# Optimization experiments

Hardware: AMD Instinct MI355X
Metric: run time of the kernel (lower is better)

The kernel has to match this reference:

```python
import jax, jax.numpy as jnp
import numpy as np

H = 64  # GRU hidden size


def _gru_scan(x_proj, m, U, b_rec):
    # x_proj: [S,B,3H] precomputed input projections (time-major); m: [S,B] bool mask
    B = x_proj.shape[1]
    h0 = jnp.zeros((B, H), x_proj.dtype)

    def step(h, inp):
        xp, mt = inp
        rec = h @ U + b_rec                       # [B,3H] (Keras reset_after=True)
        xz, xr, xh = jnp.split(xp, 3, axis=-1)
        rz, rr, rh = jnp.split(rec, 3, axis=-1)
        z = jax.nn.sigmoid(xz + rz)
        r = jax.nn.sigmoid(xr + rr)
        hh = jnp.tanh(xh + r * rh)
        hn = z * h + (1.0 - z) * hh
        hn = jnp.where(mt[:, None], hn, h)        # masked steps carry state through
        return hn, hn

    hT, hs = jax.lax.scan(step, h0, (x_proj, m))
    return hs, hT  # hs: [S,B,H], hT: [B,H]


def setup_inputs() -> dict:
    key = jax.random.key(0)
    ks = jax.random.split(key, 16)
    V, E = 50000, 25
    B, S, T = 512, 200, 10
    s = 0.05
    f32 = jnp.float32
    inp = {
        "input_batch": jax.random.randint(ks[0], (B, S, T), 0, V),
        "emb_table": jax.random.normal(ks[1], (V, E), f32) * s,
        "W_f": jax.random.normal(ks[2], (E, 3 * H), f32) * s,
        "U_f": jax.random.normal(ks[3], (H, 3 * H), f32) * s,
        "b_f": jnp.zeros((2, 3 * H), f32),
        "W_b": jax.random.normal(ks[4], (E, 3 * H), f32) * s,
        "U_b": jax.random.normal(ks[5], (H, 3 * H), f32) * s,
        "b_b": jnp.zeros((2, 3 * H), f32),
        "W_k": jax.random.normal(ks[6], (2 * H, H), f32) * s,
        "b_k": jnp.zeros((H,), f32),
        "W_q": jax.random.normal(ks[7], (H, H), f32) * s,
        "b_q": jnp.zeros((H,), f32),
        "W_e": jax.random.normal(ks[8], (H, 1), f32) * s,
        "b_e": jnp.zeros((1,), f32),
    }
    return inp


def reference(input_batch, emb_table, W_f, U_f, b_f, W_b, U_b, b_b, W_k, b_k, W_q, b_q, W_e, b_e):
    mask = input_batch != 0                                  # [B,S,T]
    emb = emb_table[input_batch]                             # [B,S,T,E]
    nm = mask.astype(emb.dtype)
    denom = nm.sum(axis=2)                                   # [B,S]
    denom = jnp.where(denom == 0, jnp.ones_like(denom), denom)
    x = (emb * nm[..., None]).sum(axis=2) / denom[..., None] # [B,S,E] masked mean over tags
    step_mask = mask[:, :, 0]                                # [B,S] GRU step mask

    xT = jnp.swapaxes(x, 0, 1)                               # [S,B,E]
    mT = jnp.swapaxes(step_mask, 0, 1)                       # [S,B]

    # forward GRU
    hs_f, hT_f = _gru_scan(xT @ W_f + b_f[0], mT, U_f, b_f[1])
    # backward GRU: reverse time, scan, reverse back
    hs_b, _ = _gru_scan((xT @ W_b + b_b[0])[::-1], mT[::-1], U_b, b_b[1])
    hs_b = hs_b[::-1]

    out = jnp.swapaxes(jnp.concatenate([hs_f, hs_b], axis=-1), 0, 1)  # [B,S,2H]

    # Bahdanau attention; query = forward final state
    keys = out @ W_k + b_k                                   # [B,S,H]
    queries = hT_f @ W_q + b_q                               # [B,H]
    e = jnp.tanh(keys + queries[:, None, :]) @ W_e + b_e     # [B,S,1]
    e = e + (1.0 - step_mask.astype(e.dtype))[..., None] * -1e9
    w = jax.nn.softmax(e, axis=1)                            # [B,S,1]
    context = (w * out).sum(axis=1)                          # [B,2H]
    return context
```

## Files before the change

### kernel.cpp

```cpp
#include <hip/hip_runtime.h>
#include <math.h>

#define BATCH 512
#define SEQ   200
#define TOK   10
#define EMB   25
#define HID   64
#define G3    192

__device__ __forceinline__ float fast_sigmoid(float t) {
    float e = __expf(-t);
    return __builtin_amdgcn_rcpf(1.f + e);
}
__device__ __forceinline__ float fast_tanh(float t) {
    float e2 = __expf(2.f * t);
    return 1.f - 2.f * __builtin_amdgcn_rcpf(e2 + 1.f);
}

__global__ __launch_bounds__(256) void emb_mean_kernel(
    const int* __restrict__ ids_g, const float* __restrict__ emb,
    float* __restrict__ x, float* __restrict__ mask)
{
    int grp  = blockIdx.x * 8 + (threadIdx.x >> 5);
    int lane = threadIdx.x & 31;
    if (grp >= BATCH * SEQ) return;
    const int* ids = ids_g + (size_t)grp * TOK;
    float acc = 0.f;
    int cnt = 0;
    #pragma unroll
    for (int t = 0; t < TOK; t++) {
        int id = ids[t];
        if (id != 0) {
            cnt++;
            if (lane < EMB) acc += emb[(size_t)id * EMB + lane];
        }
    }
    if (lane < EMB)
        x[(size_t)grp * EMB + lane] = cnt ? acc / (float)cnt : 0.f;
    if (lane == 0)
        mask[grp] = (ids[0] != 0) ? 1.f : 0.f;
}

__global__ __launch_bounds__(64, 1) void gru_kernel(
    const float* __restrict__ xg, const float* __restrict__ maskg,
    const float* __restrict__ W_f, const float* __restrict__ U_f, const float* __restrict__ b_f,
    const float* __restrict__ W_b, const float* __restrict__ U_b, const float* __restrict__ b_b,
    float* __restrict__ outg, float* __restrict__ hT)
{
    const int bidx = blockIdx.x;
    const int dir  = bidx >> 9;
    const int b    = bidx & 511;
    const int j    = threadIdx.x;

    const float* W    = dir ? W_b : W_f;
    const float* U    = dir ? U_b : U_f;
    const float* bias = dir ? b_b : b_f;

    float Uz[HID], Ur[HID], Uh[HID];
    #pragma unroll
    for (int k = 0; k < HID; k++) {
        Uz[k] = U[k * G3 + j];
        Ur[k] = U[k * G3 + HID + j];
        Uh[k] = U[k * G3 + 2 * HID + j];
    }
    float Wz[EMB], Wr[EMB], Wh[EMB];
    #pragma unroll
    for (int e = 0; e < EMB; e++) {
        Wz[e] = W[e * G3 + j];
        Wr[e] = W[e * G3 + HID + j];
        Wh[e] = W[e * G3 + 2 * HID + j];
    }
    const float bz0 = bias[j];
    const float br0 = bias[HID + j];
    const float bh0 = bias[2 * HID + j];
    const float bzr = bias[G3 + j];
    const float brr = bias[G3 + HID + j];
    const float bhr = bias[G3 + 2 * HID + j];

    __shared__ float xs[SEQ * EMB];
    __shared__ float ms[SEQ];
    __shared__ float hs[HID];

    {
        const float4* xrow4 = (const float4*)(xg + (size_t)b * (SEQ * EMB));
        float4* xs4 = (float4*)xs;
        for (int i = j; i < (SEQ * EMB) / 4; i += 64) xs4[i] = xrow4[i];
        for (int i = j; i < SEQ; i += 64) ms[i] = maskg[(size_t)b * SEQ + i];
        hs[j] = 0.f;
    }
    __syncthreads();

    float h = 0.f;
    float* orow_base = outg + (size_t)b * SEQ * (2 * HID) + dir * HID + j;

    for (int step = 0; step < SEQ; step++) {
        const int s = dir ? (SEQ - 1 - step) : step;

        const float* xr = xs + s * EMB;
        float pz = bz0, pr = br0, ph = bh0;
        #pragma unroll
        for (int e = 0; e < EMB; e++) {
            float xv = xr[e];
            pz = fmaf(xv, Wz[e], pz);
            pr = fmaf(xv, Wr[e], pr);
            ph = fmaf(xv, Wh[e], ph);
        }

        float az = bzr, ar = brr, ah = bhr;
        #pragma unroll
        for (int k = 0; k < HID; k++) {
            float hk = hs[k];
            az = fmaf(hk, Uz[k], az);
            ar = fmaf(hk, Ur[k], ar);
            ah = fmaf(hk, Uh[k], ah);
        }

        float z  = fast_sigmoid(pz + az);
        float r  = fast_sigmoid(pr + ar);
        float hh = fast_tanh(ph + r * ah);
        float hn = z * h + (1.f - z) * hh;
        hn = (ms[s] != 0.f) ? hn : h;
        h = hn;

        __builtin_amdgcn_wave_barrier();
        hs[j] = hn;
        __builtin_amdgcn_wave_barrier();

        orow_base[(size_t)s * (2 * HID)] = hn;
    }
    if (dir == 0) hT[(size_t)b * HID + j] = h;
}

__global__ __launch_bounds__(256) void attn_kernel(
    const float* __restrict__ outg, const float* __restrict__ maskg,
    const float* __restrict__ hT,
    const float* __restrict__ W_k, const float* __restrict__ b_k,
    const float* __restrict__ W_q, const float* __restrict__ b_q,
    const float* __restrict__ W_e, const float* __restrict__ b_e,
    float* __restrict__ ctx)
{
    const int b   = blockIdx.x;
    const int tid = threadIdx.x;

    __shared__ float Wks[2 * HID * HID];
    __shared__ float qs[HID];
    __shared__ float es[SEQ];

    for (int i = tid; i < 2 * HID * HID; i += 256) Wks[i] = W_k[i];
    if (tid < HID) {
        float q = b_q[tid];
        const float* hrow = hT + (size_t)b * HID;
        #pragma unroll 8
        for (int i = 0; i < HID; i++) q = fmaf(hrow[i], W_q[i * HID + tid], q);
        qs[tid] = q;
    }
    __syncthreads();

    const int wave = tid >> 6;
    const int lane = tid & 63;
    const float bk = b_k[lane];
    const float we = W_e[lane];
    const float be = b_e[0];

    for (int s = wave; s < SEQ; s += 4) {
        const float* orow = outg + ((size_t)b * SEQ + s) * (2 * HID);
        float a0 = 0.f, a1 = 0.f, a2 = 0.f, a3 = 0.f;
        #pragma unroll
        for (int i = 0; i < 2 * HID; i += 4) {
            a0 = fmaf(orow[i + 0], Wks[(i + 0) * HID + lane], a0);
            a1 = fmaf(orow[i + 1], Wks[(i + 1) * HID + lane], a1);
            a2 = fmaf(orow[i + 2], Wks[(i + 2) * HID + lane], a2);
            a3 = fmaf(orow[i + 3], Wks[(i + 3) * HID + lane], a3);
        }
        float t = tanhf(((a0 + a1) + (a2 + a3)) + bk + qs[lane]) * we;
        #pragma unroll
        for (int off = 32; off > 0; off >>= 1) t += __shfl_down(t, off);
        if (lane == 0) {
            float pen = (maskg[(size_t)b * SEQ + s] != 0.f) ? 0.f : -1e9f;
            es[s] = t + be + pen;
        }
    }
    __syncthreads();

    if (tid < 64) {
        float mx = -1e30f;
        for (int s2 = tid; s2 < SEQ; s2 += 64) mx = fmaxf(mx, es[s2]);
        #pragma unroll
        for (int off = 32; off > 0; off >>= 1) mx = fmaxf(mx, __shfl_xor(mx, off));
        float sum = 0.f;
        for (int s2 = tid; s2 < SEQ; s2 += 64) {
            float w = expf(es[s2] - mx);
            es[s2] = w;
            sum += w;
        }
        #pragma unroll
        for (int off = 32; off > 0; off >>= 1) sum += __shfl_xor(sum, off);
        float inv = 1.f / sum;
        for (int s2 = tid; s2 < SEQ; s2 += 64) es[s2] *= inv;
    }
    __syncthreads();

    if (tid < 2 * HID) {
        const int jj = tid;
        float a0 = 0.f, a1 = 0.f;
        for (int s2 = 0; s2 < SEQ; s2 += 2) {
            a0 = fmaf(es[s2],     outg[((size_t)b * SEQ + s2)     * (2 * HID) + jj], a0);
            a1 = fmaf(es[s2 + 1], outg[((size_t)b * SEQ + s2 + 1) * (2 * HID) + jj], a1);
        }
        ctx[(size_t)b * (2 * HID) + jj] = a0 + a1;
    }
}

extern "C" void kernel_launch(void* const* d_in, const int* in_sizes, int n_in,
                              void* d_out, int out_size, void* d_ws, size_t ws_size,
                              hipStream_t stream) {
    const int*   ids = (const int*)  d_in[0];
    const float* emb = (const float*)d_in[1];
    const float* W_f = (const float*)d_in[2];
    const float* U_f = (const float*)d_in[3];
    const float* b_f = (const float*)d_in[4];
    const float* W_b = (const float*)d_in[5];
    const float* U_b = (const float*)d_in[6];
    const float* b_b = (const float*)d_in[7];
    const float* W_k = (const float*)d_in[8];
    const float* b_k = (const float*)d_in[9];
    const float* W_q = (const float*)d_in[10];
    const float* b_q = (const float*)d_in[11];
    const float* W_e = (const float*)d_in[12];
    const float* b_e = (const float*)d_in[13];

    float* ws   = (float*)d_ws;
    float* x    = ws;
    float* mask = ws + 2560000;
    float* out  = ws + 2662400;
    float* hT   = ws + 15769600;

    emb_mean_kernel<<<(BATCH * SEQ) / 8, 256, 0, stream>>>(ids, emb, x, mask);
    gru_kernel<<<1024, 64, 0, stream>>>(x, mask, W_f, U_f, b_f,
                                        W_b, U_b, b_b, out, hT);
    attn_kernel<<<BATCH, 256, 0, stream>>>(out, mask, hT, W_k, b_k,
                                           W_q, b_q, W_e, b_e, (float*)d_out);
}
```

Measured before the change: 464.0 us.

## Split GRU gates across three waves per sequence with LDS barriers

The GRU kernel now uses 192 threads per block, one wave per gate (z, r, candidate). Each thread holds one column of U and W in registers instead of three, which cuts register pressure and the serial FMA chain per step. Gate activations are exchanged through shared memory using two block barriers per step. The input projection for the next step is computed after the first barrier, overlapping it with the recurrence. In exchange, every timestep pays for two workgroup barriers.

After: 435.5 us. 6.2% less time.

```diff
diff --git a/kernel.cpp b/kernel.cpp
--- a/kernel.cpp
+++ b/kernel.cpp
@@ -16,6 +16,12 @@
     float e2 = __expf(2.f * t);
     return 1.f - 2.f * __builtin_amdgcn_rcpf(e2 + 1.f);
 }
+
+#define LDS_BARRIER() do {                                   \
+    asm volatile("s_waitcnt lgkmcnt(0)" ::: "memory");       \
+    __builtin_amdgcn_s_barrier();                            \
+    asm volatile("" ::: "memory");                           \
+} while (0)
 
 __global__ __launch_bounds__(256) void emb_mean_kernel(
     const int* __restrict__ ids_g, const float* __restrict__ emb,
@@ -41,7 +47,7 @@
         mask[grp] = (ids[0] != 0) ? 1.f : 0.f;
 }
 
-__global__ __launch_bounds__(64, 1) void gru_kernel(
+__global__ __launch_bounds__(192, 3) void gru_kernel(
     const float* __restrict__ xg, const float* __restrict__ maskg,
     const float* __restrict__ W_f, const float* __restrict__ U_f, const float* __restrict__ b_f,
     const float* __restrict__ W_b, const float* __restrict__ U_b, const float* __restrict__ b_b,
@@ -50,85 +56,103 @@
     const int bidx = blockIdx.x;
     const int dir  = bidx >> 9;
     const int b    = bidx & 511;
-    const int j    = threadIdx.x;
+    const int tid  = threadIdx.x;
+    const int w    = tid >> 6;
+    const int j    = tid & 63;
 
     const float* W    = dir ? W_b : W_f;
     const float* U    = dir ? U_b : U_f;
     const float* bias = dir ? b_b : b_f;
 
-    float Uz[HID], Ur[HID], Uh[HID];
+    const int col = w * HID + j;
+
+    float Ug[HID];
     #pragma unroll
-    for (int k = 0; k < HID; k++) {
-        Uz[k] = U[k * G3 + j];
-        Ur[k] = U[k * G3 + HID + j];
-        Uh[k] = U[k * G3 + 2 * HID + j];
-    }
-    float Wz[EMB], Wr[EMB], Wh[EMB];
+    for (int k = 0; k < HID; k++) Ug[k] = U[k * G3 + col];
+    float Wg[EMB];
     #pragma unroll
-    for (int e = 0; e < EMB; e++) {
-        Wz[e] = W[e * G3 + j];
-        Wr[e] = W[e * G3 + HID + j];
-        Wh[e] = W[e * G3 + 2 * HID + j];
-    }
-    const float bz0 = bias[j];
-    const float br0 = bias[HID + j];
-    const float bh0 = bias[2 * HID + j];
-    const float bzr = bias[G3 + j];
-    const float brr = bias[G3 + HID + j];
-    const float bhr = bias[G3 + 2 * HID + j];
+    for (int e = 0; e < EMB; e++) Wg[e] = W[e * G3 + col];
+    const float bx = bias[col];
+    const float br = bias[G3 + col];
 
     __shared__ float xs[SEQ * EMB];
     __shared__ float ms[SEQ];
     __shared__ float hs[HID];
+    __shared__ float zs[HID];
+    __shared__ float rs[HID];
 
     {
         const float4* xrow4 = (const float4*)(xg + (size_t)b * (SEQ * EMB));
         float4* xs4 = (float4*)xs;
-        for (int i = j; i < (SEQ * EMB) / 4; i += 64) xs4[i] = xrow4[i];
-        for (int i = j; i < SEQ; i += 64) ms[i] = maskg[(size_t)b * SEQ + i];
-        hs[j] = 0.f;
+        for (int i = tid; i < (SEQ * EMB) / 4; i += 192) xs4[i] = xrow4[i];
+        for (int i = tid; i < SEQ; i += 192) ms[i] = maskg[(size_t)b * SEQ + i];
+        if (tid < HID) hs[tid] = 0.f;
     }
     __syncthreads();
 
     float h = 0.f;
-    float* orow_base = outg + (size_t)b * SEQ * (2 * HID) + dir * HID + j;
+    float* obase = outg + (size_t)b * SEQ * (2 * HID) + dir * HID + j;
+
+    float p;
+    {
+        const int s0 = dir ? (SEQ - 1) : 0;
+        const float* xr = xs + s0 * EMB;
+        float q0 = bx, q1 = 0.f;
+        #pragma unroll
+        for (int e = 0; e + 1 < EMB; e += 2) {
+            q0 = fmaf(xr[e],     Wg[e],     q0);
+            q1 = fmaf(xr[e + 1], Wg[e + 1], q1);
+        }
+        q0 = fmaf(xr[EMB - 1], Wg[EMB - 1], q0);
+        p = q0 + q1;
+    }
 
     for (int step = 0; step < SEQ; step++) {
         const int s = dir ? (SEQ - 1 - step) : step;
 
-        const float* xr = xs + s * EMB;
-        float pz = bz0, pr = br0, ph = bh0;
-        #pragma unroll
-        for (int e = 0; e < EMB; e++) {
-            float xv = xr[e];
-            pz = fmaf(xv, Wz[e], pz);
-            pr = fmaf(xv, Wr[e], pr);
-            ph = fmaf(xv, Wh[e], ph);
-        }
-
-        float az = bzr, ar = brr, ah = bhr;
-        #pragma unroll
-        for (int k = 0; k < HID; k++) {
-            float hk = hs[k];
-            az = fmaf(hk, Uz[k], az);
-            ar = fmaf(hk, Ur[k], ar);
-            ah = fmaf(hk, Uh[k], ah);
-        }
-
-        float z  = fast_sigmoid(pz + az);
-        float r  = fast_sigmoid(pr + ar);
-        float hh = fast_tanh(ph + r * ah);
-        float hn = z * h + (1.f - z) * hh;
-        hn = (ms[s] != 0.f) ? hn : h;
-        h = hn;
-
-        __builtin_amdgcn_wave_barrier();
-        hs[j] = hn;
-        __builtin_amdgcn_wave_barrier();
-
-        orow_base[(size_t)s * (2 * HID)] = hn;
-    }
-    if (dir == 0) hT[(size_t)b * HID + j] = h;
+        float a0 = br, a1 = 0.f, a2 = 0.f, a3 = 0.f;
+        #pragma unroll
+        for (int k = 0; k < HID; k += 4) {
+            a0 = fmaf(hs[k],     Ug[k],     a0);
+            a1 = fmaf(hs[k + 1], Ug[k + 1], a1);
+            a2 = fmaf(hs[k + 2], Ug[k + 2], a2);
+            a3 = fmaf(hs[k + 3], Ug[k + 3], a3);
+        }
+        const float a = (a0 + a1) + (a2 + a3);
+
+        if (w == 0)      zs[j] = fast_sigmoid(p + a);
+        else if (w == 1) rs[j] = fast_sigmoid(p + a);
+
+        LDS_BARRIER();
+
+        if (w == 2) {
+            float r  = rs[j];
+            float z  = zs[j];
+            float hh = fast_tanh(p + r * a);
+            float hn = z * h + (1.f - z) * hh;
+            hn = (ms[s] != 0.f) ? hn : h;
+            h = hn;
+            hs[j] = hn;
+            obase[(size_t)s * (2 * HID)] = hn;
+        }
+
+        {
+            const int sn  = dir ? (SEQ - 2 - step) : (step + 1);
+            const int snc = (step + 1 < SEQ) ? sn : s;
+            const float* xr = xs + snc * EMB;
+            float q0 = bx, q1 = 0.f;
+            #pragma unroll
+            for (int e = 0; e + 1 < EMB; e += 2) {
+                q0 = fmaf(xr[e],     Wg[e],     q0);
+                q1 = fmaf(xr[e + 1], Wg[e + 1], q1);
+            }
+            q0 = fmaf(xr[EMB - 1], Wg[EMB - 1], q0);
+            p = q0 + q1;
+        }
+
+        LDS_BARRIER();
+    }
+    if (w == 2 && dir == 0) hT[(size_t)b * HID + j] = h;
 }
 
 __global__ __launch_bounds__(256) void attn_kernel(
@@ -236,8 +260,8 @@
     float* hT   = ws + 15769600;
 
     emb_mean_kernel<<<(BATCH * SEQ) / 8, 256, 0, stream>>>(ids, emb, x, mask);
-    gru_kernel<<<1024, 64, 0, stream>>>(x, mask, W_f, U_f, b_f,
-                                        W_b, U_b, b_b, out, hT);
+    gru_kernel<<<1024, 192, 0, stream>>>(x, mask, W_f, U_f, b_f,
+                                         W_b, U_b, b_b, out, hT);
     attn_kernel<<<BATCH, 256, 0, stream>>>(out, mask, hT, W_k, b_k,
                                            W_q, b_q, W_e, b_e, (float*)d_out);
 }
```
